# Kernel optimization log

Measured on AMD Instinct MI355X. Metric: run time of the kernel, lower is better.

Reference implementation:

```python
import jax, jax.numpy as jnp
import numpy as np

V, E, U, T, B = 32000, 256, 512, 32, 64

def setup_inputs() -> dict:
    key = jax.random.key(0)
    ks = jax.random.split(key, 12)
    return {
        "input_seq": jax.random.randint(ks[0], (B, T), 1, V),
        "target": jax.random.randint(ks[1], (B, T), 1, V),
        "encoder_output": jax.random.normal(ks[2], (B, T, U), jnp.float32),
        "enc_h": jax.random.normal(ks[3], (B, U), jnp.float32),
        "enc_c": jax.random.normal(ks[4], (B, U), jnp.float32),
        "emb": jax.random.normal(ks[5], (V, E), jnp.float32) * 0.02,
        "Wk": jax.random.normal(ks[6], (E, 4 * U), jnp.float32) * 0.05,
        "Wr": jax.random.normal(ks[7], (U, 4 * U), jnp.float32) * 0.05,
        "b": jnp.zeros((4 * U,), jnp.float32),
        "Wgen": jax.random.normal(ks[8], (2 * U + E, U), jnp.float32) * 0.05,
        "bgen": jnp.zeros((U,), jnp.float32),
    }


def _lstm(x, h0, c0, Wk, Wr, b):
    # x: [B,T,E]; Keras gate order i,f,c,o; returns seq of h [B,T,U], hT, cT
    xg = jnp.einsum('bte,eg->btg', x, Wk) + b  # precompute input projections
    def cell(carry, xg_t):
        h, c = carry
        g = xg_t + h @ Wr
        i, f, cc, o = jnp.split(g, 4, axis=-1)
        c_new = jax.nn.sigmoid(f) * c + jax.nn.sigmoid(i) * jnp.tanh(cc)
        h_new = jax.nn.sigmoid(o) * jnp.tanh(c_new)
        return (h_new, c_new), h_new
    (hT, cT), hs = jax.lax.scan(cell, (h0, c0), jnp.swapaxes(xg, 0, 1))
    return jnp.swapaxes(hs, 0, 1), hT, cT


def reference(input_seq, target, encoder_output, enc_h, enc_c, emb, Wk, Wr, b, Wgen, bgen):
    dec_in0 = emb[target]  # [B,T,E]
    def outer(carry, _):
        dec_in, h, c = carry
        outs, hT, cT = _lstm(dec_in, h, c, Wk, Wr, b)  # [B,T,U]
        h_b = jnp.broadcast_to(h[:, None, :], (B, T, U))  # pre-update state, per original
        feat = jnp.concatenate([encoder_output, h_b, dec_in], axis=-1)
        p_gen = jax.nn.sigmoid(feat @ Wgen + bgen)  # [B,T,U]
        idx = jnp.argmax(outs, axis=-1)  # greedy 'token' ids (as in original)
        new_in = emb[idx]
        return (new_in, hT, cT), (outs, p_gen, h, c)
    _, (dec_outs, p_gens, hs, cs) = jax.lax.scan(
        outer, (dec_in0, enc_h, enc_c), None, length=T - 1)
    return dec_outs, p_gens, hs, cs
```

## Files before the change

kernel.cpp:

```cpp
#include <hip/hip_runtime.h>
#include <math.h>

#define Bz 64
#define Tz 32
#define Uz 512
#define NITER 31
#define G4 2048

typedef unsigned long long ull;

__device__ __forceinline__ float sigf(float x) { return 1.f / (1.f + expf(-x)); }

#define AT_LOADF(p)   __hip_atomic_load((p), __ATOMIC_RELAXED, __HIP_MEMORY_SCOPE_AGENT)
#define AT_LOADI(p)   __hip_atomic_load((p), __ATOMIC_RELAXED, __HIP_MEMORY_SCOPE_AGENT)
#define AT_LOAD64(p)  __hip_atomic_load((p), __ATOMIC_RELAXED, __HIP_MEMORY_SCOPE_AGENT)
#define AT_STORE(p,v) __hip_atomic_store((p), (v), __ATOMIC_RELAXED, __HIP_MEMORY_SCOPE_AGENT)

__device__ __forceinline__ void poll32(unsigned* fl, unsigned target) {
  int sl = threadIdx.x & 63;
  unsigned v;
  do {
    v = __hip_atomic_fetch_add(&fl[sl * 16], 0u, __ATOMIC_RELAXED, __HIP_MEMORY_SCOPE_AGENT);
  } while (__any((int)(v < target)));
}

__global__ __launch_bounds__(256) void gemm_f32(
    const float* __restrict__ A, const int* __restrict__ Arows, int lda,
    const float* __restrict__ Bm, int ldb, const float* __restrict__ bias,
    float* __restrict__ C, int N, int K)
{
  __shared__ __align__(16) float As[16][68];
  __shared__ __align__(16) float Bs[16][68];
  const int tid = threadIdx.x;
  const int bm = blockIdx.y, bn = blockIdx.x;
  const int tx = tid & 15, ty = tid >> 4;
  float acc[4][4] = {{0.f}};
  const int sm = tid >> 2, sk = (tid & 3) * 4;
  const int arow = Arows ? Arows[bm * 64 + sm] : (bm * 64 + sm);
  const float* Ap = A + (size_t)arow * lda + sk;
  const int bk = tid >> 4, bn4 = (tid & 15) * 4;
  const float* Bp = Bm + (size_t)bk * ldb + bn * 64 + bn4;
  for (int kk = 0; kk < K; kk += 16) {
    float4 av = *(const float4*)(Ap + kk);
    float4 bv = *(const float4*)(Bp + (size_t)kk * ldb);
    As[sk + 0][sm] = av.x; As[sk + 1][sm] = av.y;
    As[sk + 2][sm] = av.z; As[sk + 3][sm] = av.w;
    *(float4*)&Bs[bk][bn4] = bv;
    __syncthreads();
#pragma unroll
    for (int kt = 0; kt < 16; ++kt) {
      float4 a = *(const float4*)&As[kt][ty * 4];
      float4 b = *(const float4*)&Bs[kt][tx * 4];
      acc[0][0] += a.x * b.x; acc[0][1] += a.x * b.y; acc[0][2] += a.x * b.z; acc[0][3] += a.x * b.w;
      acc[1][0] += a.y * b.x; acc[1][1] += a.y * b.y; acc[1][2] += a.y * b.z; acc[1][3] += a.y * b.w;
      acc[2][0] += a.z * b.x; acc[2][1] += a.z * b.y; acc[2][2] += a.z * b.z; acc[2][3] += a.z * b.w;
      acc[3][0] += a.w * b.x; acc[3][1] += a.w * b.y; acc[3][2] += a.w * b.z; acc[3][3] += a.w * b.w;
    }
    __syncthreads();
  }
  const int cm = bm * 64 + ty * 4, cn = bn * 64 + tx * 4;
  float bc0 = bias ? bias[cn + 0] : 0.f;
  float bc1 = bias ? bias[cn + 1] : 0.f;
  float bc2 = bias ? bias[cn + 2] : 0.f;
  float bc3 = bias ? bias[cn + 3] : 0.f;
#pragma unroll
  for (int i = 0; i < 4; ++i) {
    float4 o;
    o.x = acc[i][0] + bc0; o.y = acc[i][1] + bc1;
    o.z = acc[i][2] + bc2; o.w = acc[i][3] + bc3;
    *(float4*)&C[(size_t)(cm + i) * N + cn] = o;
  }
}

__global__ void init_kernel(unsigned* __restrict__ flags) {
  int i = blockIdx.x * blockDim.x + threadIdx.x;
  if (i < 8192) flags[i] = 0u;
}

#define DO_GEMM(HRED, GIDX, GV)                                                          \
  {                                                                                      \
    float4 a0 = {0,0,0,0}, a1 = {0,0,0,0}, a2 = {0,0,0,0}, a3 = {0,0,0,0};               \
    _Pragma("unroll")                                                                    \
    for (int kk = 0; kk < 16; ++kk) {                                                    \
      float4 hv = *(const float4*)&HRED[(kk * 32 + ks) * 4];                             \
      a0.x += hv.x * w4[kk].x; a0.y += hv.x * w4[kk].y;                                  \
      a0.z += hv.x * w4[kk].z; a0.w += hv.x * w4[kk].w;                                  \
      a1.x += hv.y * w4[kk].x; a1.y += hv.y * w4[kk].y;                                  \
      a1.z += hv.y * w4[kk].z; a1.w += hv.y * w4[kk].w;                                  \
      a2.x += hv.z * w4[kk].x; a2.y += hv.z * w4[kk].y;                                  \
      a2.z += hv.z * w4[kk].z; a2.w += hv.z * w4[kk].w;                                  \
      a3.x += hv.w * w4[kk].x; a3.y += hv.w * w4[kk].y;                                  \
      a3.z += hv.w * w4[kk].z; a3.w += hv.w * w4[kk].w;                                  \
    }                                                                                    \
    bool c1 = ks & 1, c2 = ks & 2, c3 = ks & 4, c4 = ks & 8;                             \
    float4 k0 = c1 ? a2 : a0, k1 = c1 ? a3 : a1;                                         \
    float4 s0 = c1 ? a0 : a2, s1 = c1 ? a1 : a3;                                         \
    k0.x += __shfl_xor(s0.x, 2); k0.y += __shfl_xor(s0.y, 2);                            \
    k0.z += __shfl_xor(s0.z, 2); k0.w += __shfl_xor(s0.w, 2);                            \
    k1.x += __shfl_xor(s1.x, 2); k1.y += __shfl_xor(s1.y, 2);                            \
    k1.z += __shfl_xor(s1.z, 2); k1.w += __shfl_xor(s1.w, 2);                            \
    float4 m0 = c2 ? k1 : k0, n0 = c2 ? k0 : k1;                                         \
    m0.x += __shfl_xor(n0.x, 4); m0.y += __shfl_xor(n0.y, 4);                            \
    m0.z += __shfl_xor(n0.z, 4); m0.w += __shfl_xor(n0.w, 4);                            \
    float q0 = c3 ? m0.z : m0.x, q1 = c3 ? m0.w : m0.y;                                  \
    float r0 = c3 ? m0.x : m0.z, r1 = c3 ? m0.y : m0.w;                                  \
    q0 += __shfl_xor(r0, 8); q1 += __shfl_xor(r1, 8);                                    \
    float u_ = c4 ? q1 : q0, v_ = c4 ? q0 : q1;                                          \
    u_ += __shfl_xor(v_, 16);                                                            \
    u_ += __shfl_xor(u_, 32);                                                            \
    if (lane < 32) g_l[GIDX][b_f][j_f] = u_ + (GV);                                      \
  }

__global__ __launch_bounds__(512, 1) void decoder_persist(
    const float* __restrict__ Wr,
    const float* __restrict__ Wgen,
    const float* __restrict__ bgen,
    const float* __restrict__ enc_h,
    const float* __restrict__ enc_c,
    const float* __restrict__ embW,
    const float* __restrict__ xg0,
    const float* __restrict__ enc_part,
    const float* __restrict__ dec0,
    const float* __restrict__ decW,
    float* __restrict__ hbT,
    int*   __restrict__ idxbuf,
    unsigned* __restrict__ flags,
    float* __restrict__ out)
{
  __shared__ __align__(16) float hredA[2048];
  __shared__ __align__(16) float hredB[2048];
  __shared__ __align__(16) float Wgenl[8192];
  __shared__ float g_l[2][4][68];
  __shared__ float hW_l[128];
  __shared__ float redl[512];
  __shared__ int   idx_l[8][32];
  __shared__ float bgen_l[16];

  const int tid = threadIdx.x;
  const int bid = blockIdx.x;
  const int pr = bid >> 5, ug = bid & 31;
  const int bA0 = pr * 4, bB0 = 32 + pr * 4;
  const int u0 = ug * 16;
  const int w = tid >> 6, lane = tid & 63;
  const int ks = lane >> 1, jsub = lane & 1;
  const int jloc = w * 8 + jsub * 4;
  const int gcol0 = (jloc >> 4) * Uz + u0 + (jloc & 15);
  const int b_f = 2 * (ks & 1) + ((ks >> 1) & 1);
  const int ji_f = 2 * ((ks >> 2) & 1) + ((ks >> 3) & 1);
  const int j_f = jloc + ji_f;
  const int gcol_f = (j_f >> 4) * Uz + u0 + (j_f & 15);
  const int p_b = lane >> 4, p_ul = lane & 15;

  float* out_dec = out;
  float* out_pg  = out + (size_t)NITER * Bz * Tz * Uz;
  float* out_hs  = out + 2 * (size_t)NITER * Bz * Tz * Uz;
  float* out_cs  = out_hs + (size_t)NITER * Bz * Uz;

  unsigned* flA = flags + (pr * 2 + 0) * 512;
  unsigned* flB = flags + (pr * 2 + 1) * 512;
  float* hbTp = hbT + pr * 8192;

  float4 w4[16];
#pragma unroll
  for (int kk = 0; kk < 16; ++kk)
    w4[kk] = *(const float4*)&Wr[(size_t)(kk * 32 + ks) * G4 + gcol0];
  for (int q = 0; q < 16; ++q) {
    int e = q * 512 + tid, k = e >> 4, ul = e & 15;
    Wgenl[k * 16 + ul] = Wgen[(size_t)(512 + k) * Uz + u0 + ul];
  }
  if (tid < 16) bgen_l[tid] = bgen[u0 + tid];
  {
    int k = tid;
#pragma unroll
    for (int b = 0; b < 4; ++b) {
      hredA[k * 4 + b] = enc_h[(size_t)(bA0 + b) * Uz + k];
      hredB[k * 4 + b] = enc_h[(size_t)(bB0 + b) * Uz + k];
    }
  }
  float c_reg = 0.f;
  if (w == 0) c_reg = enc_c[(size_t)(bA0 + p_b) * Uz + u0 + p_ul];
  if (w == 1) c_reg = enc_c[(size_t)(bB0 + p_b) * Uz + u0 + p_ul];
  __syncthreads();

#pragma unroll 1
  for (int s = 0; s < NITER; ++s) {
    const int* idxp = idxbuf + ((s + 1) & 1) * 2048;
    int*       idxq = idxbuf + (s & 1) * 2048;
    const unsigned base = 33u * s;

    if (s > 0) {
      if (w == 1 && lane < 32) poll32(flA, base);
      __syncthreads();
      if (tid < 128) {
        int pb = tid >> 4, t2 = (tid & 15) * 2;
        int batch = (pb < 4) ? bA0 + pb : bB0 + (pb - 4);
        idx_l[pb][t2]     = AT_LOADI(&idxp[batch * Tz + t2]);
        idx_l[pb][t2 + 1] = AT_LOADI(&idxp[batch * Tz + t2 + 1]);
      } else if (w >= 2 && w < 6) {
        int st = tid - 128;
        const ull* src = (const ull*)&hbTp[1 * 2048];
        ull* dst = (ull*)hredB;
#pragma unroll
        for (int q = 0; q < 4; ++q) dst[q * 256 + st] = AT_LOAD64(&src[q * 256 + st]);
      }
      __syncthreads();
    }
    {
      int g = tid >> 8, r6 = tid & 255, kq = r6 >> 6, l6 = r6 & 63;
      int b = l6 >> 4, ul = l6 & 15;
      const float* hr = g ? hredB : hredA;
      float a = 0.f;
#pragma unroll 8
      for (int k = kq * 128; k < kq * 128 + 128; ++k)
        a += hr[k * 4 + b] * Wgenl[k * 16 + ul];
      redl[tid] = a;
    }
    __syncthreads();
    if (tid < 128) {
      int g = tid >> 6, l6 = tid & 63;
      hW_l[tid] = (redl[g * 256 + l6] + redl[g * 256 + 64 + l6]) +
                  (redl[g * 256 + 128 + l6] + redl[g * 256 + 192 + l6]);
    }
    if (w < 2) {
      int batch = (w == 0 ? bA0 : bB0) + p_b;
      const float* hr = w ? hredB : hredA;
      out_hs[((size_t)s * Bz + batch) * Uz + u0 + p_ul] = hr[(u0 + p_ul) * 4 + p_b];
      out_cs[((size_t)s * Bz + batch) * Uz + u0 + p_ul] = c_reg;
    }
    __syncthreads();
#pragma unroll 1
    for (int i = 0; i < 8; ++i) {
      int o = i * 512 + tid;
      int ul = o & 15, t = (o >> 4) & 31, pb = o >> 9;
      int batch = (pb < 4) ? bA0 + pb : bB0 + (pb - 4);
      size_t r = (size_t)batch * Tz + t;
      float dv = (s == 0) ? dec0[r * Uz + u0 + ul]
                          : decW[(size_t)idx_l[pb][t] * Uz + u0 + ul];
      float v = enc_part[r * Uz + u0 + ul] + hW_l[(pb >> 2) * 64 + (pb & 3) * 16 + ul]
              + dv + bgen_l[ul];
      out_pg[(((size_t)s * Bz + batch) * Tz + t) * Uz + u0 + ul] = sigf(v);
    }

#pragma unroll 1
    for (int t = 0; t < Tz; ++t) {
      const int gt = s * Tz + t;
      ull stg[16];
      float gvA = 0.f, gvB = 0.f;
      if (lane < 32) {
        int rA = (bA0 + b_f) * Tz + t, rB = (bB0 + b_f) * Tz + t;
        if (s == 0) {
          gvA = xg0[(size_t)rA * G4 + gcol_f];
          gvB = xg0[(size_t)rB * G4 + gcol_f];
        } else {
          gvA = embW[(size_t)idx_l[b_f][t] * G4 + gcol_f];
          gvB = embW[(size_t)idx_l[4 + b_f][t] * G4 + gcol_f];
        }
      }
      if (w == 1 && gt > 0) {
        if (lane < 32) poll32(flB, base + t);
        const ull* src = (const ull*)&hbTp[((gt & 1) * 2 + 1) * 2048];
#pragma unroll
        for (int q = 0; q < 16; ++q) stg[q] = AT_LOAD64(&src[q * 64 + lane]);
      }
      DO_GEMM(hredA, 0, gvA);
      __syncthreads();
      if (w == 0) {
        float gi = g_l[0][p_b][p_ul],      gf = g_l[0][p_b][16 + p_ul];
        float gc = g_l[0][p_b][32 + p_ul], go = g_l[0][p_b][48 + p_ul];
        c_reg = sigf(gf) * c_reg + sigf(gi) * tanhf(gc);
        float hn = sigf(go) * tanhf(c_reg);
        int parw = (gt + 1) & 1;
        AT_STORE(&hbTp[(parw * 2 + 0) * 2048 + (u0 + p_ul) * 4 + p_b], hn);
        AT_STORE(&out_dec[(((size_t)s * Bz + bA0 + p_b) * Tz + t) * Uz + u0 + p_ul], hn);
        asm volatile("s_waitcnt vmcnt(0)" ::: "memory");
        if (lane == 0) AT_STORE(&flA[ug * 16], base + t + 1);
      } else if (w == 1 && gt > 0) {
        ull* dst = (ull*)hredB;
#pragma unroll
        for (int q = 0; q < 16; ++q) dst[q * 64 + lane] = stg[q];
      }
      __syncthreads();
      if (w == 6) {
        if (lane < 32) poll32(flA, base + t + 1);
        const ull* src = (const ull*)&hbTp[(((gt + 1) & 1) * 2 + 0) * 2048];
#pragma unroll
        for (int q = 0; q < 16; ++q) stg[q] = AT_LOAD64(&src[q * 64 + lane]);
      }
      DO_GEMM(hredB, 1, gvB);
      __syncthreads();
      if (w == 1) {
        float gi = g_l[1][p_b][p_ul],      gf = g_l[1][p_b][16 + p_ul];
        float gc = g_l[1][p_b][32 + p_ul], go = g_l[1][p_b][48 + p_ul];
        c_reg = sigf(gf) * c_reg + sigf(gi) * tanhf(gc);
        float hn = sigf(go) * tanhf(c_reg);
        int parw = (gt + 1) & 1;
        AT_STORE(&hbTp[(parw * 2 + 1) * 2048 + (u0 + p_ul) * 4 + p_b], hn);
        AT_STORE(&out_dec[(((size_t)s * Bz + bB0 + p_b) * Tz + t) * Uz + u0 + p_ul], hn);
        asm volatile("s_waitcnt vmcnt(0)" ::: "memory");
        if (lane == 0) AT_STORE(&flB[ug * 16], base + t + 1);
      } else if (w == 6) {
        ull* dst = (ull*)hredA;
#pragma unroll
        for (int q = 0; q < 16; ++q) dst[q * 64 + lane] = stg[q];
      }
      __syncthreads();
    }

    if (s < NITER - 1) {
      if (w == 1 && lane < 32) poll32(flB, base + 32);
      __syncthreads();
      {
        int R = ug * 8 + w;
        int pb = R >> 5, t = R & 31;
        int batch = (pb < 4) ? bA0 + pb : bB0 + (pb - 4);
        const float* row = &out_dec[(((size_t)s * Bz + batch) * Tz + t) * Uz];
        float bv = -3.4e38f; int bi = 0;
#pragma unroll
        for (int q = 0; q < 8; ++q) {
          int u = lane + q * 64;
          float v = AT_LOADF(&row[u]);
          if (v > bv) { bv = v; bi = u; }
        }
#pragma unroll
        for (int off = 1; off < 64; off <<= 1) {
          float ov = __shfl_xor(bv, off);
          int   oi = __shfl_xor(bi, off);
          if (ov > bv || (ov == bv && oi < bi)) { bv = ov; bi = oi; }
        }
        if (lane == 0) AT_STORE(&idxq[batch * Tz + t], bi);
      }
      asm volatile("s_waitcnt vmcnt(0)" ::: "memory");
      __syncthreads();
      if (tid == 0) {
        AT_STORE(&flA[ug * 16], base + 33);
        AT_STORE(&flB[ug * 16], base + 33);
      }
    }
  }
}

extern "C" void kernel_launch(void* const* d_in, const int* in_sizes, int n_in,
                              void* d_out, int out_size, void* d_ws, size_t ws_size,
                              hipStream_t stream) {
  const int*   target = (const int*)d_in[1];
  const float* enc    = (const float*)d_in[2];
  const float* enc_h  = (const float*)d_in[3];
  const float* enc_cp = (const float*)d_in[4];
  const float* emb    = (const float*)d_in[5];
  const float* Wk     = (const float*)d_in[6];
  const float* Wr     = (const float*)d_in[7];
  const float* bb     = (const float*)d_in[8];
  const float* Wgen   = (const float*)d_in[9];
  const float* bgen   = (const float*)d_in[10];
  float* out = (float*)d_out;

  float* ws = (float*)d_ws;
  float* hbT      = ws;
  float* embW     = ws + 65536;
  float* xg0      = ws + 1114112;
  float* enc_part = ws + 5308416;
  float* dec0     = ws + 6356992;
  float* decW     = ws + 7405568;
  int*   idxbuf   = (int*)(ws + 7667712);
  unsigned* flags = (unsigned*)(ws + 7671808);

  init_kernel<<<16, 512, 0, stream>>>(flags);
  gemm_f32<<<dim3(32, 8), 256, 0, stream>>>(emb, nullptr, 256, Wk, 2048, bb, embW, 2048, 256);
  gemm_f32<<<dim3(32, 32), 256, 0, stream>>>(emb, target, 256, Wk, 2048, bb, xg0, 2048, 256);
  gemm_f32<<<dim3(8, 32), 256, 0, stream>>>(enc, nullptr, 512, Wgen, 512, nullptr, enc_part, 512, 512);
  gemm_f32<<<dim3(8, 32), 256, 0, stream>>>(emb, target, 256, Wgen + 1024 * 512, 512, nullptr, dec0, 512, 256);
  gemm_f32<<<dim3(8, 8), 256, 0, stream>>>(emb, nullptr, 256, Wgen + 1024 * 512, 512, nullptr, decW, 512, 256);

  decoder_persist<<<256, 512, 0, stream>>>(Wr, Wgen, bgen, enc_h, enc_cp, embW, xg0,
      enc_part, dec0, decW, hbT, idxbuf, flags, out);
}
```

Baseline: 5.794 ms.

## Split persistent LSTM decoder across twice as many blocks with two batches each

```diff
diff --git a/kernel.cpp b/kernel.cpp
--- a/kernel.cpp
+++ b/kernel.cpp
@@ -74,44 +74,35 @@
 
 __global__ void init_kernel(unsigned* __restrict__ flags) {
   int i = blockIdx.x * blockDim.x + threadIdx.x;
-  if (i < 8192) flags[i] = 0u;
-}
-
-#define DO_GEMM(HRED, GIDX, GV)                                                          \
-  {                                                                                      \
-    float4 a0 = {0,0,0,0}, a1 = {0,0,0,0}, a2 = {0,0,0,0}, a3 = {0,0,0,0};               \
-    _Pragma("unroll")                                                                    \
-    for (int kk = 0; kk < 16; ++kk) {                                                    \
-      float4 hv = *(const float4*)&HRED[(kk * 32 + ks) * 4];                             \
-      a0.x += hv.x * w4[kk].x; a0.y += hv.x * w4[kk].y;                                  \
-      a0.z += hv.x * w4[kk].z; a0.w += hv.x * w4[kk].w;                                  \
-      a1.x += hv.y * w4[kk].x; a1.y += hv.y * w4[kk].y;                                  \
-      a1.z += hv.y * w4[kk].z; a1.w += hv.y * w4[kk].w;                                  \
-      a2.x += hv.z * w4[kk].x; a2.y += hv.z * w4[kk].y;                                  \
-      a2.z += hv.z * w4[kk].z; a2.w += hv.z * w4[kk].w;                                  \
-      a3.x += hv.w * w4[kk].x; a3.y += hv.w * w4[kk].y;                                  \
-      a3.z += hv.w * w4[kk].z; a3.w += hv.w * w4[kk].w;                                  \
-    }                                                                                    \
-    bool c1 = ks & 1, c2 = ks & 2, c3 = ks & 4, c4 = ks & 8;                             \
-    float4 k0 = c1 ? a2 : a0, k1 = c1 ? a3 : a1;                                         \
-    float4 s0 = c1 ? a0 : a2, s1 = c1 ? a1 : a3;                                         \
-    k0.x += __shfl_xor(s0.x, 2); k0.y += __shfl_xor(s0.y, 2);                            \
-    k0.z += __shfl_xor(s0.z, 2); k0.w += __shfl_xor(s0.w, 2);                            \
-    k1.x += __shfl_xor(s1.x, 2); k1.y += __shfl_xor(s1.y, 2);                            \
-    k1.z += __shfl_xor(s1.z, 2); k1.w += __shfl_xor(s1.w, 2);                            \
-    float4 m0 = c2 ? k1 : k0, n0 = c2 ? k0 : k1;                                         \
-    m0.x += __shfl_xor(n0.x, 4); m0.y += __shfl_xor(n0.y, 4);                            \
-    m0.z += __shfl_xor(n0.z, 4); m0.w += __shfl_xor(n0.w, 4);                            \
-    float q0 = c3 ? m0.z : m0.x, q1 = c3 ? m0.w : m0.y;                                  \
-    float r0 = c3 ? m0.x : m0.z, r1 = c3 ? m0.y : m0.w;                                  \
-    q0 += __shfl_xor(r0, 8); q1 += __shfl_xor(r1, 8);                                    \
-    float u_ = c4 ? q1 : q0, v_ = c4 ? q0 : q1;                                          \
-    u_ += __shfl_xor(v_, 16);                                                            \
-    u_ += __shfl_xor(u_, 32);                                                            \
-    if (lane < 32) g_l[GIDX][b_f][j_f] = u_ + (GV);                                      \
-  }
-
-__global__ __launch_bounds__(512, 1) void decoder_persist(
+  if (i < 16384) flags[i] = 0u;
+}
+
+#define DO_GEMM(HRED, GIDX, GV)                                             \
+  {                                                                         \
+    float4 a0 = {0,0,0,0}, a1 = {0,0,0,0};                                  \
+    _Pragma("unroll")                                                       \
+    for (int kk = 0; kk < 16; ++kk) {                                       \
+      float2 hv = *(const float2*)&HRED[(kk * 32 + ks) * 2];                \
+      a0.x += hv.x * w4[kk].x; a0.y += hv.x * w4[kk].y;                     \
+      a0.z += hv.x * w4[kk].z; a0.w += hv.x * w4[kk].w;                     \
+      a1.x += hv.y * w4[kk].x; a1.y += hv.y * w4[kk].y;                     \
+      a1.z += hv.y * w4[kk].z; a1.w += hv.y * w4[kk].w;                     \
+    }                                                                       \
+    bool c1 = ks & 1, c2 = ks & 2, c3 = ks & 4;                             \
+    float4 K = c1 ? a1 : a0, S = c1 ? a0 : a1;                              \
+    K.x += __shfl_xor(S.x, 2); K.y += __shfl_xor(S.y, 2);                   \
+    K.z += __shfl_xor(S.z, 2); K.w += __shfl_xor(S.w, 2);                   \
+    float m0 = c2 ? K.z : K.x, m1 = c2 ? K.w : K.y;                         \
+    float n0 = c2 ? K.x : K.z, n1 = c2 ? K.y : K.w;                         \
+    m0 += __shfl_xor(n0, 4); m1 += __shfl_xor(n1, 4);                       \
+    float q_ = c3 ? m1 : m0, r_ = c3 ? m0 : m1;                             \
+    q_ += __shfl_xor(r_, 8);                                                \
+    q_ += __shfl_xor(q_, 16);                                               \
+    q_ += __shfl_xor(q_, 32);                                               \
+    if (lane < 16) g_l[GIDX][b_f][j_f] = q_ + (GV);                         \
+  }
+
+__global__ __launch_bounds__(512, 4) void decoder_persist(
     const float* __restrict__ Wr,
     const float* __restrict__ Wgen,
     const float* __restrict__ bgen,
@@ -127,29 +118,28 @@
     unsigned* __restrict__ flags,
     float* __restrict__ out)
 {
-  __shared__ __align__(16) float hredA[2048];
-  __shared__ __align__(16) float hredB[2048];
+  __shared__ __align__(16) float hredA[1024];
+  __shared__ __align__(16) float hredB[1024];
   __shared__ __align__(16) float Wgenl[8192];
-  __shared__ float g_l[2][4][68];
-  __shared__ float hW_l[128];
+  __shared__ float g_l[2][2][68];
+  __shared__ float hW_l[64];
   __shared__ float redl[512];
-  __shared__ int   idx_l[8][32];
+  __shared__ int   idx_l[4][32];
   __shared__ float bgen_l[16];
 
   const int tid = threadIdx.x;
   const int bid = blockIdx.x;
-  const int pr = bid >> 5, ug = bid & 31;
-  const int bA0 = pr * 4, bB0 = 32 + pr * 4;
+  const int pr = (bid >> 5) & 15, ug = bid & 31;
+  const int bA0 = pr * 2, bB0 = 32 + pr * 2;
   const int u0 = ug * 16;
   const int w = tid >> 6, lane = tid & 63;
   const int ks = lane >> 1, jsub = lane & 1;
   const int jloc = w * 8 + jsub * 4;
   const int gcol0 = (jloc >> 4) * Uz + u0 + (jloc & 15);
-  const int b_f = 2 * (ks & 1) + ((ks >> 1) & 1);
-  const int ji_f = 2 * ((ks >> 2) & 1) + ((ks >> 3) & 1);
-  const int j_f = jloc + ji_f;
+  const int b_f = ks & 1;
+  const int j_f = jloc + 2 * ((ks >> 1) & 1) + ((ks >> 2) & 1);
   const int gcol_f = (j_f >> 4) * Uz + u0 + (j_f & 15);
-  const int p_b = lane >> 4, p_ul = lane & 15;
+  const int p_b = (lane >> 4) & 1, p_ul = lane & 15;
 
   float* out_dec = out;
   float* out_pg  = out + (size_t)NITER * Bz * Tz * Uz;
@@ -158,7 +148,7 @@
 
   unsigned* flA = flags + (pr * 2 + 0) * 512;
   unsigned* flB = flags + (pr * 2 + 1) * 512;
-  float* hbTp = hbT + pr * 8192;
+  float* hbTp = hbT + pr * 4096;
 
   float4 w4[16];
 #pragma unroll
@@ -171,15 +161,14 @@
   if (tid < 16) bgen_l[tid] = bgen[u0 + tid];
   {
     int k = tid;
-#pragma unroll
-    for (int b = 0; b < 4; ++b) {
-      hredA[k * 4 + b] = enc_h[(size_t)(bA0 + b) * Uz + k];
-      hredB[k * 4 + b] = enc_h[(size_t)(bB0 + b) * Uz + k];
-    }
+    hredA[k * 2 + 0] = enc_h[(size_t)(bA0 + 0) * Uz + k];
+    hredA[k * 2 + 1] = enc_h[(size_t)(bA0 + 1) * Uz + k];
+    hredB[k * 2 + 0] = enc_h[(size_t)(bB0 + 0) * Uz + k];
+    hredB[k * 2 + 1] = enc_h[(size_t)(bB0 + 1) * Uz + k];
   }
   float c_reg = 0.f;
-  if (w == 0) c_reg = enc_c[(size_t)(bA0 + p_b) * Uz + u0 + p_ul];
-  if (w == 1) c_reg = enc_c[(size_t)(bB0 + p_b) * Uz + u0 + p_ul];
+  if (w == 0 && lane < 32) c_reg = enc_c[(size_t)(bA0 + p_b) * Uz + u0 + p_ul];
+  if (w == 1 && lane < 32) c_reg = enc_c[(size_t)(bB0 + p_b) * Uz + u0 + p_ul];
   __syncthreads();
 
 #pragma unroll 1
@@ -192,51 +181,55 @@
       if (w == 1 && lane < 32) poll32(flA, base);
       __syncthreads();
       if (tid < 128) {
-        int pb = tid >> 4, t2 = (tid & 15) * 2;
-        int batch = (pb < 4) ? bA0 + pb : bB0 + (pb - 4);
-        idx_l[pb][t2]     = AT_LOADI(&idxp[batch * Tz + t2]);
-        idx_l[pb][t2 + 1] = AT_LOADI(&idxp[batch * Tz + t2 + 1]);
+        int pb = tid >> 5, t = tid & 31;
+        int batch = (pb < 2) ? bA0 + pb : bB0 + (pb - 2);
+        idx_l[pb][t] = AT_LOADI(&idxp[batch * Tz + t]);
       } else if (w >= 2 && w < 6) {
         int st = tid - 128;
-        const ull* src = (const ull*)&hbTp[1 * 2048];
+        const ull* src = (const ull*)&hbTp[1 * 1024];
         ull* dst = (ull*)hredB;
 #pragma unroll
-        for (int q = 0; q < 4; ++q) dst[q * 256 + st] = AT_LOAD64(&src[q * 256 + st]);
+        for (int q = 0; q < 2; ++q) dst[q * 256 + st] = AT_LOAD64(&src[q * 256 + st]);
       }
       __syncthreads();
     }
     {
-      int g = tid >> 8, r6 = tid & 255, kq = r6 >> 6, l6 = r6 & 63;
-      int b = l6 >> 4, ul = l6 & 15;
+      int g = tid >> 8, r = tid & 255;
+      int kp = r >> 5, b = (r >> 4) & 1, ul = r & 15;
       const float* hr = g ? hredB : hredA;
       float a = 0.f;
 #pragma unroll 8
-      for (int k = kq * 128; k < kq * 128 + 128; ++k)
-        a += hr[k * 4 + b] * Wgenl[k * 16 + ul];
+      for (int k = kp * 64; k < kp * 64 + 64; ++k)
+        a += hr[k * 2 + b] * Wgenl[k * 16 + ul];
       redl[tid] = a;
     }
     __syncthreads();
-    if (tid < 128) {
-      int g = tid >> 6, l6 = tid & 63;
-      hW_l[tid] = (redl[g * 256 + l6] + redl[g * 256 + 64 + l6]) +
-                  (redl[g * 256 + 128 + l6] + redl[g * 256 + 192 + l6]);
-    }
-    if (w < 2) {
-      int batch = (w == 0 ? bA0 : bB0) + p_b;
-      const float* hr = w ? hredB : hredA;
-      out_hs[((size_t)s * Bz + batch) * Uz + u0 + p_ul] = hr[(u0 + p_ul) * 4 + p_b];
+    if (tid < 64) {
+      int g = tid >> 5, r = tid & 31;
+      float a = 0.f;
+#pragma unroll
+      for (int kp = 0; kp < 8; ++kp) a += redl[g * 256 + kp * 32 + r];
+      hW_l[tid] = a;
+    }
+    if (w == 0 && lane < 32) {
+      int batch = bA0 + p_b;
+      out_hs[((size_t)s * Bz + batch) * Uz + u0 + p_ul] = hredA[(u0 + p_ul) * 2 + p_b];
+      out_cs[((size_t)s * Bz + batch) * Uz + u0 + p_ul] = c_reg;
+    } else if (w == 1 && lane < 32) {
+      int batch = bB0 + p_b;
+      out_hs[((size_t)s * Bz + batch) * Uz + u0 + p_ul] = hredB[(u0 + p_ul) * 2 + p_b];
       out_cs[((size_t)s * Bz + batch) * Uz + u0 + p_ul] = c_reg;
     }
     __syncthreads();
 #pragma unroll 1
-    for (int i = 0; i < 8; ++i) {
+    for (int i = 0; i < 4; ++i) {
       int o = i * 512 + tid;
       int ul = o & 15, t = (o >> 4) & 31, pb = o >> 9;
-      int batch = (pb < 4) ? bA0 + pb : bB0 + (pb - 4);
+      int batch = (pb < 2) ? bA0 + pb : bB0 + (pb - 2);
       size_t r = (size_t)batch * Tz + t;
       float dv = (s == 0) ? dec0[r * Uz + u0 + ul]
                           : decW[(size_t)idx_l[pb][t] * Uz + u0 + ul];
-      float v = enc_part[r * Uz + u0 + ul] + hW_l[(pb >> 2) * 64 + (pb & 3) * 16 + ul]
+      float v = enc_part[r * Uz + u0 + ul] + hW_l[(pb >> 1) * 32 + (pb & 1) * 16 + ul]
               + dv + bgen_l[ul];
       out_pg[(((size_t)s * Bz + batch) * Tz + t) * Uz + u0 + ul] = sigf(v);
     }
@@ -244,64 +237,68 @@
 #pragma unroll 1
     for (int t = 0; t < Tz; ++t) {
       const int gt = s * Tz + t;
-      ull stg[16];
+      ull stg[8];
       float gvA = 0.f, gvB = 0.f;
-      if (lane < 32) {
+      if (lane < 16) {
         int rA = (bA0 + b_f) * Tz + t, rB = (bB0 + b_f) * Tz + t;
         if (s == 0) {
           gvA = xg0[(size_t)rA * G4 + gcol_f];
           gvB = xg0[(size_t)rB * G4 + gcol_f];
         } else {
           gvA = embW[(size_t)idx_l[b_f][t] * G4 + gcol_f];
-          gvB = embW[(size_t)idx_l[4 + b_f][t] * G4 + gcol_f];
+          gvB = embW[(size_t)idx_l[2 + b_f][t] * G4 + gcol_f];
         }
       }
       if (w == 1 && gt > 0) {
         if (lane < 32) poll32(flB, base + t);
-        const ull* src = (const ull*)&hbTp[((gt & 1) * 2 + 1) * 2048];
-#pragma unroll
-        for (int q = 0; q < 16; ++q) stg[q] = AT_LOAD64(&src[q * 64 + lane]);
+        const ull* src = (const ull*)&hbTp[((gt & 1) * 2 + 1) * 1024];
+#pragma unroll
+        for (int q = 0; q < 8; ++q) stg[q] = AT_LOAD64(&src[q * 64 + lane]);
       }
       DO_GEMM(hredA, 0, gvA);
       __syncthreads();
-      if (w == 0) {
+      if (w == 0 && lane < 32) {
         float gi = g_l[0][p_b][p_ul],      gf = g_l[0][p_b][16 + p_ul];
         float gc = g_l[0][p_b][32 + p_ul], go = g_l[0][p_b][48 + p_ul];
         c_reg = sigf(gf) * c_reg + sigf(gi) * tanhf(gc);
         float hn = sigf(go) * tanhf(c_reg);
         int parw = (gt + 1) & 1;
-        AT_STORE(&hbTp[(parw * 2 + 0) * 2048 + (u0 + p_ul) * 4 + p_b], hn);
+        AT_STORE(&hbTp[(parw * 2 + 0) * 1024 + (u0 + p_ul) * 2 + p_b], hn);
         AT_STORE(&out_dec[(((size_t)s * Bz + bA0 + p_b) * Tz + t) * Uz + u0 + p_ul], hn);
+      }
+      if (w == 0) {
         asm volatile("s_waitcnt vmcnt(0)" ::: "memory");
-        if (lane == 0) AT_STORE(&flA[ug * 16], base + t + 1);
+        if (tid == 0) AT_STORE(&flA[ug * 16], base + t + 1);
       } else if (w == 1 && gt > 0) {
         ull* dst = (ull*)hredB;
 #pragma unroll
-        for (int q = 0; q < 16; ++q) dst[q * 64 + lane] = stg[q];
+        for (int q = 0; q < 8; ++q) dst[q * 64 + lane] = stg[q];
       }
       __syncthreads();
       if (w == 6) {
         if (lane < 32) poll32(flA, base + t + 1);
-        const ull* src = (const ull*)&hbTp[(((gt + 1) & 1) * 2 + 0) * 2048];
-#pragma unroll
-        for (int q = 0; q < 16; ++q) stg[q] = AT_LOAD64(&src[q * 64 + lane]);
+        const ull* src = (const ull*)&hbTp[(((gt + 1) & 1) * 2 + 0) * 1024];
+#pragma unroll
+        for (int q = 0; q < 8; ++q) stg[q] = AT_LOAD64(&src[q * 64 + lane]);
       }
       DO_GEMM(hredB, 1, gvB);
       __syncthreads();
-      if (w == 1) {
+      if (w == 1 && lane < 32) {
         float gi = g_l[1][p_b][p_ul],      gf = g_l[1][p_b][16 + p_ul];
         float gc = g_l[1][p_b][32 + p_ul], go = g_l[1][p_b][48 + p_ul];
         c_reg = sigf(gf) * c_reg + sigf(gi) * tanhf(gc);
         float hn = sigf(go) * tanhf(c_reg);
         int parw = (gt + 1) & 1;
-        AT_STORE(&hbTp[(parw * 2 + 1) * 2048 + (u0 + p_ul) * 4 + p_b], hn);
+        AT_STORE(&hbTp[(parw * 2 + 1) * 1024 + (u0 + p_ul) * 2 + p_b], hn);
         AT_STORE(&out_dec[(((size_t)s * Bz + bB0 + p_b) * Tz + t) * Uz + u0 + p_ul], hn);
+      }
+      if (w == 1) {
         asm volatile("s_waitcnt vmcnt(0)" ::: "memory");
         if (lane == 0) AT_STORE(&flB[ug * 16], base + t + 1);
       } else if (w == 6) {
         ull* dst = (ull*)hredA;
 #pragma unroll
-        for (int q = 0; q < 16; ++q) dst[q * 64 + lane] = stg[q];
+        for (int q = 0; q < 8; ++q) dst[q * 64 + lane] = stg[q];
       }
       __syncthreads();
     }
@@ -309,10 +306,10 @@
     if (s < NITER - 1) {
       if (w == 1 && lane < 32) poll32(flB, base + 32);
       __syncthreads();
-      {
-        int R = ug * 8 + w;
+      if (w < 4) {
+        int R = ug * 4 + w;
         int pb = R >> 5, t = R & 31;
-        int batch = (pb < 4) ? bA0 + pb : bB0 + (pb - 4);
+        int batch = (pb < 2) ? bA0 + pb : bB0 + (pb - 2);
         const float* row = &out_dec[(((size_t)s * Bz + batch) * Tz + t) * Uz];
         float bv = -3.4e38f; int bi = 0;
 #pragma unroll
@@ -364,13 +361,13 @@
   int*   idxbuf   = (int*)(ws + 7667712);
   unsigned* flags = (unsigned*)(ws + 7671808);
 
-  init_kernel<<<16, 512, 0, stream>>>(flags);
+  init_kernel<<<32, 512, 0, stream>>>(flags);
   gemm_f32<<<dim3(32, 8), 256, 0, stream>>>(emb, nullptr, 256, Wk, 2048, bb, embW, 2048, 256);
   gemm_f32<<<dim3(32, 32), 256, 0, stream>>>(emb, target, 256, Wk, 2048, bb, xg0, 2048, 256);
   gemm_f32<<<dim3(8, 32), 256, 0, stream>>>(enc, nullptr, 512, Wgen, 512, nullptr, enc_part, 512, 512);
   gemm_f32<<<dim3(8, 32), 256, 0, stream>>>(emb, target, 256, Wgen + 1024 * 512, 512, nullptr, dec0, 512, 256);
   gemm_f32<<<dim3(8, 8), 256, 0, stream>>>(emb, nullptr, 256, Wgen + 1024 * 512, 512, nullptr, decW, 512, 256);
 
-  decoder_persist<<<256, 512, 0, stream>>>(Wr, Wgen, bgen, enc_h, enc_cp, embW, xg0,
+  decoder_persist<<<512, 512, 0, stream>>>(Wr, Wgen, bgen, enc_h, enc_cp, embW, xg0,
       enc_part, dec0, decW, hbT, idxbuf, flags, out);
 }
```

New measurement: 6.832 ms. 17.9% more time.
